# Kernel tuning notes

Measured on AMD Instinct MI355X. Metric: run time of the kernel, lower is better.

Reference implementation:

```python
import jax, jax.numpy as jnp
import numpy as np

N_HEAD = 16
N_KV_HEAD = 4
HEAD_DIM = 128  # n_embd // n_head = 2048 // 16


def _apply_rope(x, pos, T):
    # x: [B, H, T, D]; RoPE cache built exactly like the torch module:
    # cos/sin use repeat_interleave(2) on freqs, rotation uses half-split.
    D = x.shape[-1]
    half = D // 2
    inv_freq = 1.0 / jnp.power(10000.0, jnp.arange(0, D, 2, dtype=jnp.float32) / D)  # [half]
    t = jnp.arange(pos, pos + T, dtype=jnp.float32)                                  # [T]
    freqs = t[:, None] * inv_freq[None, :]                                           # [T, half]
    freqs = jnp.repeat(freqs, 2, axis=-1)                                            # [T, D]
    cos = jnp.cos(freqs)[None, None, :, :]
    sin = jnp.sin(freqs)[None, None, :, :]
    x1, x2 = x[..., :half], x[..., half:]
    rotated = jnp.concatenate([-x2, x1], axis=-1)
    return x * cos + rotated * sin


def setup_inputs() -> dict:
    key = jax.random.key(0)
    ks = jax.random.split(key, 5)
    B, T, E = 2, 2048, 2048
    KV = N_KV_HEAD * HEAD_DIM  # 512
    s = 0.02
    return {
        "x": jax.random.normal(ks[0], (B, T, E), dtype=jnp.float32),
        "Wq": jax.random.normal(ks[1], (E, E), dtype=jnp.float32) * s,
        "Wk": jax.random.normal(ks[2], (E, KV), dtype=jnp.float32) * s,
        "Wv": jax.random.normal(ks[3], (E, KV), dtype=jnp.float32) * s,
        "Wproj": jax.random.normal(ks[4], (E, E), dtype=jnp.float32) * s,
        "pos": 0,
    }


def reference(x, Wq, Wk, Wv, Wproj, pos):
    B, T, E = x.shape
    H, HKV, D = N_HEAD, N_KV_HEAD, HEAD_DIM
    G = H // HKV  # query heads per kv head

    q = (x @ Wq).reshape(B, T, H, D).transpose(0, 2, 1, 3)     # [B,H,T,D]
    k = (x @ Wk).reshape(B, T, HKV, D).transpose(0, 2, 1, 3)   # [B,HKV,T,D]
    v = (x @ Wv).reshape(B, T, HKV, D).transpose(0, 2, 1, 3)   # [B,HKV,T,D]

    q = _apply_rope(q, pos, T)
    k = _apply_rope(k, pos, T)

    # GQA: group query heads over shared kv heads
    qg = q.reshape(B, HKV, G, T, D)
    scale = 1.0 / jnp.sqrt(jnp.asarray(D, dtype=x.dtype))
    scores = jnp.einsum('bkgtd,bksd->bkgts', qg, k) * scale    # [B,HKV,G,T,T]

    causal = jnp.tril(jnp.ones((T, T), dtype=bool))
    scores = jnp.where(causal, scores, jnp.finfo(scores.dtype).min)
    attn = jax.nn.softmax(scores, axis=-1)

    out = jnp.einsum('bkgts,bksd->bkgtd', attn, v)             # [B,HKV,G,T,D]
    y = out.reshape(B, H, T, D).transpose(0, 2, 1, 3).reshape(B, T, E)
    return y @ Wproj
```

## Files before the change

### kernel.cpp

```cpp
#include <hip/hip_runtime.h>
#include <hip/hip_bf16.h>
#include <stdint.h>

typedef unsigned short u16;
typedef float f32x4 __attribute__((ext_vector_type(4)));
typedef __bf16 bf16x8 __attribute__((ext_vector_type(8)));
typedef unsigned short u16x8 __attribute__((ext_vector_type(8)));
typedef unsigned short u16x4 __attribute__((ext_vector_type(4)));
typedef float f32x4v __attribute__((ext_vector_type(4)));

#define T_SEQ 2048

__device__ __forceinline__ u16 f2bf(float f) {
    unsigned int u = __float_as_uint(f);
    unsigned int r = (u + 0x7fffu + ((u >> 16) & 1u)) >> 16;
    return (u16)r;
}
__device__ __forceinline__ float bf2f(u16 b) {
    return __uint_as_float(((unsigned int)b) << 16);
}

__device__ __forceinline__ void gload_lds16(const void* g, void* l) {
    __builtin_amdgcn_global_load_lds(
        (__attribute__((address_space(1))) void*)(g),
        (__attribute__((address_space(3))) void*)(l), 16, 0, 0);
}

__global__ void prep_all(const float* __restrict__ x, u16* __restrict__ xbf,
                         const float* __restrict__ Wq, const float* __restrict__ Wk,
                         const float* __restrict__ Wv, const float* __restrict__ Wp,
                         u16* __restrict__ WtQKV, u16* __restrict__ WtP) {
    __shared__ alignas(16) float sW[64 * 68];
    const int t = threadIdx.x;
    const int bid = blockIdx.x;
    if (bid < 4096) {
        int i = bid * 256 + t;
        const f32x4v* p = (const f32x4v*)(x + (size_t)i * 8);
        f32x4v a = p[0], bb = p[1];
        u16x8 v;
        v[0]=f2bf(a.x); v[1]=f2bf(a.y); v[2]=f2bf(a.z); v[3]=f2bf(a.w);
        v[4]=f2bf(bb.x); v[5]=f2bf(bb.y); v[6]=f2bf(bb.z); v[7]=f2bf(bb.w);
        *(u16x8*)(xbf + (size_t)i * 8) = v;
        return;
    }
    const int rem = bid - 4096;
    const int y = rem >> 5;
    const float* W; u16* dst; int N; int n0;
    if (y < 32)      { W = Wq; dst = WtQKV;                       N = 2048; n0 = y * 64; }
    else if (y < 40) { W = Wk; dst = WtQKV + (size_t)2048 * 2048; N = 512;  n0 = (y - 32) * 64; }
    else if (y < 48) { W = Wv; dst = WtQKV + (size_t)2560 * 2048; N = 512;  n0 = (y - 40) * 64; }
    else             { W = Wp; dst = WtP;                         N = 2048; n0 = (y - 48) * 64; }
    const int k0 = (rem & 31) * 64;
#pragma unroll
    for (int i = 0; i < 4; i++) {
        int kr = i * 16 + (t >> 4), nc = (t & 15) * 4;
        *(f32x4v*)&sW[kr * 68 + nc] = *(const f32x4v*)&W[(size_t)(k0 + kr) * N + n0 + nc];
    }
    __syncthreads();
#pragma unroll
    for (int i = 0; i < 2; i++) {
        int nr = i * 32 + (t >> 3), kc = (t & 7) * 8;
        u16x8 v;
#pragma unroll
        for (int j = 0; j < 8; j++) v[j] = f2bf(sW[(kc + j) * 68 + nr]);
        *(u16x8*)&dst[(size_t)(n0 + nr) * 2048 + k0 + kc] = v;
    }
}

__device__ __forceinline__ void stage_rows(const u16* g, u16* lds, int R, int kcol0, int K, int t) {
    int row = R + (t >> 3);
    int u = t & 7;
    gload_lds16(g + (size_t)row * K + kcol0 + ((u ^ (row & 7)) * 8), lds + row * 64 + u * 8);
}
__device__ __forceinline__ void stage_half256(const u16* g, u16* lds, int half, int j, int kcol0, int K, int t) {
    int idx = j * 512 + t;
    int group = idx >> 8;
    int r32 = (idx >> 3) & 31;
    int row = group * 64 + half * 32 + r32;
    int u = idx & 7;
    gload_lds16(g + (size_t)row * K + kcol0 + ((u ^ (row & 7)) * 8), lds + row * 64 + u * 8);
}
__device__ __forceinline__ bf16x8 lds_ld(const u16* lds, int row, int kc, int hl) {
    return *(const bf16x8*)&lds[row * 64 + (((kc * 4 + hl) ^ (row & 7)) * 8)];
}

__global__ __launch_bounds__(512, 2) void gemm_qkv(const u16* __restrict__ A, const u16* __restrict__ Bt,
                                                   u16* __restrict__ C, int M, int N, int K) {
    __shared__ alignas(16) u16 ldsA[2][256 * 64];
    __shared__ alignas(16) u16 ldsB[2][192 * 64];
    const int t = threadIdx.x, wave = t >> 6, lane = t & 63;
    const int l15 = lane & 15, hl = lane >> 4;
    const int wr = wave >> 2, wc = wave & 3;

    const int f = blockIdx.x;
    const int swz = (f & 7) * 32 + (f >> 3);
    const int bx = swz & 15, by = swz >> 4;
    const int m0 = bx * 256, n0 = by * 192;

    const u16* gA = A + (size_t)m0 * K;
    const u16* gB = Bt + (size_t)n0 * K;

    f32x4 acc[8][3];
    f32x4 z = {0.f, 0.f, 0.f, 0.f};
#pragma unroll
    for (int m = 0; m < 8; m++)
#pragma unroll
        for (int n = 0; n < 3; n++) acc[m][n] = z;

    stage_rows(gA, ldsA[0], 0, 0, K, t);
    stage_rows(gA, ldsA[0], 128, 0, K, t);
    stage_rows(gB, ldsB[0], 0, 0, K, t);
    stage_rows(gB, ldsB[0], 64, 0, K, t);
    stage_rows(gB, ldsB[0], 128, 0, K, t);
    stage_rows(gA, ldsA[0], 64, 0, K, t);
    stage_rows(gA, ldsA[0], 192, 0, K, t);

    const int KT = K >> 6;
    for (int kt = 0; kt < KT; ++kt) {
        const int c = kt & 1;
        const int kn = (kt + 1 < KT) ? (kt + 1) * 64 : kt * 64;
        const u16* lAc = ldsA[c];
        const u16* lBc = ldsB[c];
        u16* lAn = ldsA[c ^ 1];
        u16* lBn = ldsB[c ^ 1];

        bf16x8 aF[4][2], bF[3][2];

        asm volatile("s_waitcnt vmcnt(2)" ::: "memory");
        __builtin_amdgcn_s_barrier();
#pragma unroll
        for (int mi = 0; mi < 4; mi++)
#pragma unroll
            for (int kc = 0; kc < 2; kc++)
                aF[mi][kc] = lds_ld(lAc, wr * 128 + mi * 16 + l15, kc, hl);
#pragma unroll
        for (int n = 0; n < 3; n++)
#pragma unroll
            for (int kc = 0; kc < 2; kc++)
                bF[n][kc] = lds_ld(lBc, wc * 48 + n * 16 + l15, kc, hl);
        stage_rows(gA, lAn, 0, kn, K, t);
        stage_rows(gA, lAn, 128, kn, K, t);
        stage_rows(gB, lBn, 0, kn, K, t);
        __builtin_amdgcn_s_setprio(1);
#pragma unroll
        for (int mi = 0; mi < 4; mi++)
#pragma unroll
            for (int n = 0; n < 3; n++)
#pragma unroll
                for (int kc = 0; kc < 2; kc++)
                    acc[mi][n] = __builtin_amdgcn_mfma_f32_16x16x32_bf16(aF[mi][kc], bF[n][kc], acc[mi][n], 0, 0, 0);
        __builtin_amdgcn_s_setprio(0);

        asm volatile("s_waitcnt vmcnt(3)" ::: "memory");
        __builtin_amdgcn_s_barrier();
#pragma unroll
        for (int mi = 0; mi < 4; mi++)
#pragma unroll
            for (int kc = 0; kc < 2; kc++)
                aF[mi][kc] = lds_ld(lAc, wr * 128 + 64 + mi * 16 + l15, kc, hl);
        stage_rows(gB, lBn, 64, kn, K, t);
        stage_rows(gB, lBn, 128, kn, K, t);
        stage_rows(gA, lAn, 64, kn, K, t);
        stage_rows(gA, lAn, 192, kn, K, t);
        __builtin_amdgcn_s_setprio(1);
#pragma unroll
        for (int mi = 0; mi < 4; mi++)
#pragma unroll
            for (int n = 0; n < 3; n++)
#pragma unroll
                for (int kc = 0; kc < 2; kc++)
                    acc[4 + mi][n] = __builtin_amdgcn_mfma_f32_16x16x32_bf16(aF[mi][kc], bF[n][kc], acc[4 + mi][n], 0, 0, 0);
        __builtin_amdgcn_s_setprio(0);
    }

#pragma unroll
    for (int m = 0; m < 8; m++)
#pragma unroll
        for (int n = 0; n < 3; n++)
#pragma unroll
            for (int r = 0; r < 4; r++) {
                int row = m0 + wr * 128 + m * 16 + hl * 4 + r;
                int col = n0 + wc * 48 + n * 16 + l15;
                C[(size_t)row * N + col] = f2bf(acc[m][n][r]);
            }
}

__global__ __launch_bounds__(512, 2) void gemm_proj(const u16* __restrict__ A, const u16* __restrict__ Bt,
                                                    float* __restrict__ C, int M, int N, int K) {
    __shared__ alignas(16) u16 ldsA[2][128 * 64];
    __shared__ alignas(16) u16 ldsB[2][256 * 64];
    const int t = threadIdx.x, wave = t >> 6, lane = t & 63;
    const int l15 = lane & 15, hl = lane >> 4;
    const int wr = wave >> 2, wc = wave & 3;

    const int f = blockIdx.x;
    const int swz = (f & 7) * 32 + (f >> 3);
    const int bx = swz & 31, by = swz >> 5;
    const int m0 = bx * 128, n0 = by * 256;

    const u16* gA = A + (size_t)m0 * K;
    const u16* gB = Bt + (size_t)n0 * K;

    f32x4 acc[4][4];
    f32x4 z = {0.f, 0.f, 0.f, 0.f};
#pragma unroll
    for (int m = 0; m < 4; m++)
#pragma unroll
        for (int n = 0; n < 4; n++) acc[m][n] = z;

    stage_rows(gA, ldsA[0], 0, 0, K, t);
    stage_rows(gA, ldsA[0], 64, 0, K, t);
    stage_half256(gB, ldsB[0], 0, 0, 0, K, t);
    stage_half256(gB, ldsB[0], 0, 1, 0, K, t);
    stage_half256(gB, ldsB[0], 1, 0, 0, K, t);
    stage_half256(gB, ldsB[0], 1, 1, 0, K, t);

    const int KT = K >> 6;
    for (int kt = 0; kt < KT; ++kt) {
        const int c = kt & 1;
        const int kn = (kt + 1 < KT) ? (kt + 1) * 64 : kt * 64;
        const u16* lAc = ldsA[c];
        const u16* lBc = ldsB[c];
        u16* lAn = ldsA[c ^ 1];
        u16* lBn = ldsB[c ^ 1];

        bf16x8 aF[4][2], bF[2][2];

        asm volatile("s_waitcnt vmcnt(2)" ::: "memory");
        __builtin_amdgcn_s_barrier();
#pragma unroll
        for (int mi = 0; mi < 4; mi++)
#pragma unroll
            for (int kc = 0; kc < 2; kc++)
                aF[mi][kc] = lds_ld(lAc, wr * 64 + mi * 16 + l15, kc, hl);
#pragma unroll
        for (int n = 0; n < 2; n++)
#pragma unroll
            for (int kc = 0; kc < 2; kc++)
                bF[n][kc] = lds_ld(lBc, wc * 64 + n * 16 + l15, kc, hl);
        stage_rows(gA, lAn, 0, kn, K, t);
        stage_rows(gA, lAn, 64, kn, K, t);
        stage_half256(gB, lBn, 0, 0, kn, K, t);
        stage_half256(gB, lBn, 0, 1, kn, K, t);
        __builtin_amdgcn_s_setprio(1);
#pragma unroll
        for (int mi = 0; mi < 4; mi++)
#pragma unroll
            for (int n = 0; n < 2; n++)
#pragma unroll
                for (int kc = 0; kc < 2; kc++)
                    acc[mi][n] = __builtin_amdgcn_mfma_f32_16x16x32_bf16(aF[mi][kc], bF[n][kc], acc[mi][n], 0, 0, 0);
        __builtin_amdgcn_s_setprio(0);

        asm volatile("s_waitcnt vmcnt(4)" ::: "memory");
        __builtin_amdgcn_s_barrier();
#pragma unroll
        for (int n = 0; n < 2; n++)
#pragma unroll
            for (int kc = 0; kc < 2; kc++)
                bF[n][kc] = lds_ld(lBc, wc * 64 + 32 + n * 16 + l15, kc, hl);
        stage_half256(gB, lBn, 1, 0, kn, K, t);
        stage_half256(gB, lBn, 1, 1, kn, K, t);
        __builtin_amdgcn_s_setprio(1);
#pragma unroll
        for (int mi = 0; mi < 4; mi++)
#pragma unroll
            for (int n = 0; n < 2; n++)
#pragma unroll
                for (int kc = 0; kc < 2; kc++)
                    acc[mi][2 + n] = __builtin_amdgcn_mfma_f32_16x16x32_bf16(aF[mi][kc], bF[n][kc], acc[mi][2 + n], 0, 0, 0);
        __builtin_amdgcn_s_setprio(0);
    }

#pragma unroll
    for (int m = 0; m < 4; m++)
#pragma unroll
        for (int n = 0; n < 4; n++)
#pragma unroll
            for (int r = 0; r < 4; r++) {
                int row = m0 + wr * 64 + m * 16 + hl * 4 + r;
                int col = n0 + wc * 64 + n * 16 + l15;
                C[(size_t)row * N + col] = acc[m][n][r];
            }
}

__global__ void rope_vtrans(u16* __restrict__ qkv, u16* __restrict__ vt,
                            const int* __restrict__ pos) {
    __shared__ alignas(16) u16 sT[64 * 72];
    const int t = threadIdx.x;
    if (blockIdx.x < 512) {
        const int f = blockIdx.x;
        const int t0 = (f & 31) * 64;
        const int d0 = ((f >> 5) & 1) * 64;
        const int kh = (f >> 6) & 3, b = f >> 8;
#pragma unroll
        for (int i = 0; i < 2; i++) {
            int tr = i * 32 + (t >> 3), dc = (t & 7) * 8;
            *(u16x8*)&sT[tr * 72 + dc] =
                *(const u16x8*)&qkv[(size_t)(b * T_SEQ + t0 + tr) * 3072 + 2560 + kh * 128 + d0 + dc];
        }
        __syncthreads();
#pragma unroll
        for (int i = 0; i < 2; i++) {
            int dr = i * 32 + (t >> 3), tc = (t & 7) * 8;
            u16x8 v;
#pragma unroll
            for (int j = 0; j < 8; j++) v[j] = sT[(tc + j) * 72 + dr];
            *(u16x8*)&vt[((size_t)(b * 4 + kh) * 128 + d0 + dr) * 2048 + t0 + tc] = v;
        }
    } else {
        int tid = (blockIdx.x - 512) * 256 + t;
        int j4 = tid & 15;
        int rest = tid >> 4;
        int slice = rest % 20;
        int row = rest / 20;
        if (row >= 2 * T_SEQ) return;
        float tpos = (float)((row % T_SEQ) + pos[0]);
        int base = (slice < 16) ? slice * 128 : 2048 + (slice - 16) * 128;
        u16* p = qkv + (size_t)row * 3072 + base + j4 * 4;
        u16x4 lo = *(const u16x4*)p;
        u16x4 hi = *(const u16x4*)(p + 64);
        const float c0 = 0.20762050593045702f;
        u16x4 olo, ohi;
#pragma unroll
        for (int e = 0; e < 4; e++) {
            int i = (j4 * 4 + e) >> 1;
            float fA = tpos * exp2f(-(float)i * c0);
            float fB = tpos * exp2f(-(float)(32 + i) * c0);
            float x1 = bf2f(lo[e]), x2 = bf2f(hi[e]);
            olo[e] = f2bf(x1 * cosf(fA) - x2 * sinf(fA));
            ohi[e] = f2bf(x2 * cosf(fB) + x1 * sinf(fB));
        }
        *(u16x4*)p = olo;
        *(u16x4*)(p + 64) = ohi;
    }
}

__global__ __launch_bounds__(512, 4) void attn(const u16* __restrict__ qkv,
                                               const u16* __restrict__ vt,
                                               u16* __restrict__ out) {
    __shared__ alignas(16) u16 sK[2][8192];
    __shared__ alignas(16) u16 sV[8192];
    __shared__ alignas(16) __bf16 sP[128 * 72];
    const int t = threadIdx.x, wave = t >> 6, lane = t & 63;
    const int l15 = lane & 15, hl = lane >> 4;

    const int f = blockIdx.x;
    const int sel = f >> 8, u = f & 255;
    const int bkh = u & 7, b = bkh >> 2, kh = bkh & 3;
    const int h = kh * 4 + ((u >> 3) & 3);
    const int j = u >> 5;
    const int a = sel ? (15 - j) : j;
    const int q0 = a * 128;
    const int nt = 2 * a + 2;

    const float sc = 0.08838834764831845f;

    bf16x8 qf[4];
#pragma unroll
    for (int c = 0; c < 4; c++) {
        const u16* qp = qkv + (size_t)(b * T_SEQ + q0 + wave * 16 + l15) * 3072
                        + h * 128 + c * 32 + hl * 8;
        u16x8 raw = *(const u16x8*)qp;
        u16x8 sv_;
#pragma unroll
        for (int e = 0; e < 8; e++) sv_[e] = f2bf(bf2f(raw[e]) * sc);
        qf[c] = *(bf16x8*)&sv_;
    }

    u16x8 onesu;
#pragma unroll
    for (int e = 0; e < 8; e++) onesu[e] = 0x3F80;
    const bf16x8 onesf = *(bf16x8*)&onesu;

    float mrow[4];
    f32x4 o[8];
    f32x4 osum;
    f32x4 z = {0.f, 0.f, 0.f, 0.f};
#pragma unroll
    for (int r = 0; r < 4; r++) mrow[r] = -1e30f;
    osum = z;
#pragma unroll
    for (int n8 = 0; n8 < 8; n8++) o[n8] = z;

    asm volatile("s_waitcnt vmcnt(0)" ::: "memory");

    const u16* kgbase = qkv + (size_t)(b * T_SEQ) * 3072 + 2048 + kh * 128;
    const u16* vgbase = vt + (size_t)(b * 4 + kh) * 128 * 2048;

#pragma unroll
    for (int p = 0; p < 2; p++) {
        int i = p * 512 + t;
        int row = i >> 4, c = i & 15;
        gload_lds16(kgbase + (size_t)row * 3072 + ((c ^ (row & 7)) * 8), (u16*)sK[0] + i * 8);
    }

    int cur = 0;
    for (int it = 0; it < nt; ++it) {
        const int kv0 = it * 64;
        const int kvn = (it + 1 < nt) ? kv0 + 64 : kv0;
#pragma unroll
        for (int p = 0; p < 2; p++) {
            int i = p * 512 + t;
            int row = i >> 3, c = i & 7;
            gload_lds16(vgbase + (size_t)row * 2048 + kv0 + ((c ^ (row & 7)) * 8), sV + i * 8);
        }
#pragma unroll
        for (int p = 0; p < 2; p++) {
            int i = p * 512 + t;
            int row = i >> 4, c = i & 15;
            gload_lds16(kgbase + (size_t)(kvn + row) * 3072 + ((c ^ (row & 7)) * 8),
                        (u16*)sK[cur ^ 1] + i * 8);
        }
        asm volatile("s_waitcnt vmcnt(4)" ::: "memory");
        __builtin_amdgcn_s_barrier();

        f32x4 sA[4];
#pragma unroll
        for (int n = 0; n < 4; n++) sA[n] = z;
#pragma unroll
        for (int n = 0; n < 4; n++)
#pragma unroll
            for (int c = 0; c < 4; c++) {
                int row = n * 16 + l15;
                bf16x8 kf = *(const bf16x8*)&sK[cur][row * 128 + (((c * 4 + hl) ^ (row & 7)) * 8)];
                sA[n] = __builtin_amdgcn_mfma_f32_16x16x32_bf16(qf[c], kf, sA[n], 0, 0, 0);
            }

        const bool full = (kv0 + 63 <= q0 + wave * 16);
        if (full) {
#pragma unroll
            for (int r = 0; r < 4; r++) {
                float pmax = fmaxf(fmaxf(sA[0][r], sA[1][r]), fmaxf(sA[2][r], sA[3][r]));
                if (__builtin_expect(__any(pmax > mrow[r] + 8.f), 0)) {
                    float mx = pmax;
#pragma unroll
                    for (int off = 1; off < 16; off <<= 1) mx = fmaxf(mx, __shfl_xor(mx, off));
                    float mnew = fmaxf(mrow[r], mx);
                    float alpha = __expf(mrow[r] - mnew);
                    mrow[r] = mnew;
#pragma unroll
                    for (int n8 = 0; n8 < 8; n8++) o[n8][r] *= alpha;
                    osum[r] *= alpha;
                }
#pragma unroll
                for (int n = 0; n < 4; n++)
                    sP[(wave * 16 + hl * 4 + r) * 72 + n * 16 + l15] =
                        (__bf16)__expf(sA[n][r] - mrow[r]);
            }
        } else {
#pragma unroll
            for (int r = 0; r < 4; r++) {
                const int grow = q0 + wave * 16 + hl * 4 + r;
                float mv[4];
#pragma unroll
                for (int n = 0; n < 4; n++)
                    mv[n] = (kv0 + n * 16 + l15 <= grow) ? sA[n][r] : -1e30f;
                float pmax = fmaxf(fmaxf(mv[0], mv[1]), fmaxf(mv[2], mv[3]));
                if (__builtin_expect(__any(pmax > mrow[r] + 8.f), 0)) {
                    float mx = pmax;
#pragma unroll
                    for (int off = 1; off < 16; off <<= 1) mx = fmaxf(mx, __shfl_xor(mx, off));
                    float mnew = fmaxf(mrow[r], mx);
                    float alpha = __expf(mrow[r] - mnew);
                    mrow[r] = mnew;
#pragma unroll
                    for (int n8 = 0; n8 < 8; n8++) o[n8][r] *= alpha;
                    osum[r] *= alpha;
                }
#pragma unroll
                for (int n = 0; n < 4; n++)
                    sP[(wave * 16 + hl * 4 + r) * 72 + n * 16 + l15] =
                        (__bf16)__expf(mv[n] - mrow[r]);
            }
        }

        asm volatile("s_waitcnt vmcnt(2)" ::: "memory");
        __builtin_amdgcn_s_barrier();

        bf16x8 pa[2];
#pragma unroll
        for (int k2 = 0; k2 < 2; k2++)
            pa[k2] = *(const bf16x8*)&sP[(wave * 16 + l15) * 72 + k2 * 32 + hl * 8];
#pragma unroll
        for (int k2 = 0; k2 < 2; k2++)
            osum = __builtin_amdgcn_mfma_f32_16x16x32_bf16(pa[k2], onesf, osum, 0, 0, 0);
#pragma unroll
        for (int n8 = 0; n8 < 8; n8++)
#pragma unroll
            for (int k2 = 0; k2 < 2; k2++) {
                int d = n8 * 16 + l15;
                bf16x8 vf = *(const bf16x8*)&sV[d * 64 + (((k2 * 4 + hl) ^ (d & 7)) * 8)];
                o[n8] = __builtin_amdgcn_mfma_f32_16x16x32_bf16(pa[k2], vf, o[n8], 0, 0, 0);
            }
        __builtin_amdgcn_s_barrier();
        cur ^= 1;
    }

#pragma unroll
    for (int r = 0; r < 4; r++) {
        float inv = 1.f / osum[r];
        int orow = b * T_SEQ + q0 + wave * 16 + hl * 4 + r;
#pragma unroll
        for (int n8 = 0; n8 < 8; n8++)
            out[(size_t)orow * 2048 + h * 128 + n8 * 16 + l15] = f2bf(o[n8][r] * inv);
    }
}

extern "C" void kernel_launch(void* const* d_in, const int* in_sizes, int n_in,
                              void* d_out, int out_size, void* d_ws, size_t ws_size,
                              hipStream_t stream) {
    const float* x  = (const float*)d_in[0];
    const float* Wq = (const float*)d_in[1];
    const float* Wk = (const float*)d_in[2];
    const float* Wv = (const float*)d_in[3];
    const float* Wp = (const float*)d_in[4];
    const int*   pos = (const int*)d_in[5];

    char* ws = (char*)d_ws;
    u16* xbf   = (u16*)(ws);
    u16* WtQKV = (u16*)(ws + 16777216);
    u16* WtP   = (u16*)(ws + 29360128);
    u16* QKV   = (u16*)(ws + 37748736);
    u16* Vt    = (u16*)(ws + 62914560);
    u16* AO    = (u16*)(ws + 67108864);

    prep_all<<<4096 + 2560, 256, 0, stream>>>(x, xbf, Wq, Wk, Wv, Wp, WtQKV, WtP);
    gemm_qkv<<<256, 512, 0, stream>>>(xbf, WtQKV, QKV, 4096, 3072, 2048);
    rope_vtrans<<<512 + 5120, 256, 0, stream>>>(QKV, Vt, pos);
    attn<<<512, 512, 0, stream>>>(QKV, Vt, AO);
    gemm_proj<<<256, 512, 0, stream>>>(AO, WtP, (float*)d_out, 4096, 2048, 2048);
}
```

Baseline: 183.0 us.

## Halve attention tile sizes to 64 query rows and 32 KV columns per block

```diff
diff --git a/kernel.cpp b/kernel.cpp
--- a/kernel.cpp
+++ b/kernel.cpp
@@ -336,12 +336,12 @@
     }
 }
 
-__global__ __launch_bounds__(512, 4) void attn(const u16* __restrict__ qkv,
+__global__ __launch_bounds__(256, 4) void attn(const u16* __restrict__ qkv,
                                                const u16* __restrict__ vt,
                                                u16* __restrict__ out) {
-    __shared__ alignas(16) u16 sK[2][8192];
-    __shared__ alignas(16) u16 sV[8192];
-    __shared__ alignas(16) __bf16 sP[128 * 72];
+    __shared__ alignas(16) u16 sK[2][32 * 128];
+    __shared__ alignas(16) u16 sV[64 * 64];
+    __shared__ alignas(16) __bf16 sP[64 * 40];
     const int t = threadIdx.x, wave = t >> 6, lane = t & 63;
     const int l15 = lane & 15, hl = lane >> 4;
 
@@ -350,8 +350,8 @@
     const int bkh = u & 7, b = bkh >> 2, kh = bkh & 3;
     const int h = kh * 4 + ((u >> 3) & 3);
     const int j = u >> 5;
-    const int a = sel ? (15 - j) : j;
-    const int q0 = a * 128;
+    const int a = (sel == 0) ? j : (sel == 1) ? (15 - j) : (sel == 2) ? (16 + j) : (31 - j);
+    const int q0 = a * 64;
     const int nt = 2 * a + 2;
 
     const float sc = 0.08838834764831845f;
@@ -390,24 +390,26 @@
 
 #pragma unroll
     for (int p = 0; p < 2; p++) {
-        int i = p * 512 + t;
+        int i = p * 256 + t;
         int row = i >> 4, c = i & 15;
         gload_lds16(kgbase + (size_t)row * 3072 + ((c ^ (row & 7)) * 8), (u16*)sK[0] + i * 8);
     }
 
     int cur = 0;
     for (int it = 0; it < nt; ++it) {
-        const int kv0 = it * 64;
-        const int kvn = (it + 1 < nt) ? kv0 + 64 : kv0;
+        const int kv0 = it * 32;
+        const int kvn = (it + 1 < nt) ? kv0 + 32 : kv0;
 #pragma unroll
         for (int p = 0; p < 2; p++) {
-            int i = p * 512 + t;
-            int row = i >> 3, c = i & 7;
-            gload_lds16(vgbase + (size_t)row * 2048 + kv0 + ((c ^ (row & 7)) * 8), sV + i * 8);
+            int i = p * 256 + t;
+            int line = i >> 3, qq = i & 7;
+            int s = qq ^ (line & 7);
+            int dd = line * 2 + (s >> 2), cc = s & 3;
+            gload_lds16(vgbase + (size_t)dd * 2048 + kv0 + cc * 8, sV + i * 8);
         }
 #pragma unroll
         for (int p = 0; p < 2; p++) {
-            int i = p * 512 + t;
+            int i = p * 256 + t;
             int row = i >> 4, c = i & 15;
             gload_lds16(kgbase + (size_t)(kvn + row) * 3072 + ((c ^ (row & 7)) * 8),
                         (u16*)sK[cur ^ 1] + i * 8);
@@ -415,11 +417,11 @@
         asm volatile("s_waitcnt vmcnt(4)" ::: "memory");
         __builtin_amdgcn_s_barrier();
 
-        f32x4 sA[4];
-#pragma unroll
-        for (int n = 0; n < 4; n++) sA[n] = z;
-#pragma unroll
-        for (int n = 0; n < 4; n++)
+        f32x4 sA[2];
+#pragma unroll
+        for (int n = 0; n < 2; n++) sA[n] = z;
+#pragma unroll
+        for (int n = 0; n < 2; n++)
 #pragma unroll
             for (int c = 0; c < 4; c++) {
                 int row = n * 16 + l15;
@@ -427,11 +429,11 @@
                 sA[n] = __builtin_amdgcn_mfma_f32_16x16x32_bf16(qf[c], kf, sA[n], 0, 0, 0);
             }
 
-        const bool full = (kv0 + 63 <= q0 + wave * 16);
+        const bool full = (kv0 + 31 <= q0 + wave * 16);
         if (full) {
 #pragma unroll
             for (int r = 0; r < 4; r++) {
-                float pmax = fmaxf(fmaxf(sA[0][r], sA[1][r]), fmaxf(sA[2][r], sA[3][r]));
+                float pmax = fmaxf(sA[0][r], sA[1][r]);
                 if (__builtin_expect(__any(pmax > mrow[r] + 8.f), 0)) {
                     float mx = pmax;
 #pragma unroll
@@ -444,19 +446,19 @@
                     osum[r] *= alpha;
                 }
 #pragma unroll
-                for (int n = 0; n < 4; n++)
-                    sP[(wave * 16 + hl * 4 + r) * 72 + n * 16 + l15] =
+                for (int n = 0; n < 2; n++)
+                    sP[(wave * 16 + hl * 4 + r) * 40 + n * 16 + l15] =
                         (__bf16)__expf(sA[n][r] - mrow[r]);
             }
         } else {
 #pragma unroll
             for (int r = 0; r < 4; r++) {
                 const int grow = q0 + wave * 16 + hl * 4 + r;
-                float mv[4];
-#pragma unroll
-                for (int n = 0; n < 4; n++)
+                float mv[2];
+#pragma unroll
+                for (int n = 0; n < 2; n++)
                     mv[n] = (kv0 + n * 16 + l15 <= grow) ? sA[n][r] : -1e30f;
-                float pmax = fmaxf(fmaxf(mv[0], mv[1]), fmaxf(mv[2], mv[3]));
+                float pmax = fmaxf(mv[0], mv[1]);
                 if (__builtin_expect(__any(pmax > mrow[r] + 8.f), 0)) {
                     float mx = pmax;
 #pragma unroll
@@ -469,8 +471,8 @@
                     osum[r] *= alpha;
                 }
 #pragma unroll
-                for (int n = 0; n < 4; n++)
-                    sP[(wave * 16 + hl * 4 + r) * 72 + n * 16 + l15] =
+                for (int n = 0; n < 2; n++)
+                    sP[(wave * 16 + hl * 4 + r) * 40 + n * 16 + l15] =
                         (__bf16)__expf(mv[n] - mrow[r]);
             }
         }
@@ -478,21 +480,15 @@
         asm volatile("s_waitcnt vmcnt(2)" ::: "memory");
         __builtin_amdgcn_s_barrier();
 
-        bf16x8 pa[2];
-#pragma unroll
-        for (int k2 = 0; k2 < 2; k2++)
-            pa[k2] = *(const bf16x8*)&sP[(wave * 16 + l15) * 72 + k2 * 32 + hl * 8];
-#pragma unroll
-        for (int k2 = 0; k2 < 2; k2++)
-            osum = __builtin_amdgcn_mfma_f32_16x16x32_bf16(pa[k2], onesf, osum, 0, 0, 0);
-#pragma unroll
-        for (int n8 = 0; n8 < 8; n8++)
-#pragma unroll
-            for (int k2 = 0; k2 < 2; k2++) {
-                int d = n8 * 16 + l15;
-                bf16x8 vf = *(const bf16x8*)&sV[d * 64 + (((k2 * 4 + hl) ^ (d & 7)) * 8)];
-                o[n8] = __builtin_amdgcn_mfma_f32_16x16x32_bf16(pa[k2], vf, o[n8], 0, 0, 0);
-            }
+        bf16x8 pa = *(const bf16x8*)&sP[(wave * 16 + l15) * 40 + hl * 8];
+        osum = __builtin_amdgcn_mfma_f32_16x16x32_bf16(pa, onesf, osum, 0, 0, 0);
+#pragma unroll
+        for (int n8 = 0; n8 < 8; n8++) {
+            int d = n8 * 16 + l15;
+            int line = d >> 1;
+            bf16x8 vf = *(const bf16x8*)&sV[line * 64 + ((((d & 1) * 4 + hl) ^ (line & 7)) * 8)];
+            o[n8] = __builtin_amdgcn_mfma_f32_16x16x32_bf16(pa, vf, o[n8], 0, 0, 0);
+        }
         __builtin_amdgcn_s_barrier();
         cur ^= 1;
     }
@@ -528,6 +524,6 @@
     prep_all<<<4096 + 2560, 256, 0, stream>>>(x, xbf, Wq, Wk, Wv, Wp, WtQKV, WtP);
     gemm_qkv<<<256, 512, 0, stream>>>(xbf, WtQKV, QKV, 4096, 3072, 2048);
     rope_vtrans<<<512 + 5120, 256, 0, stream>>>(QKV, Vt, pos);
-    attn<<<512, 512, 0, stream>>>(QKV, Vt, AO);
+    attn<<<1024, 256, 0, stream>>>(QKV, Vt, AO);
     gemm_proj<<<256, 512, 0, stream>>>(AO, WtP, (float*)d_out, 4096, 2048, 2048);
 }
```

After: 192.0 us. +4.9%, slower.
